# Kernel tuning notes

Hardware: AMD Instinct MI355X
Metric: run time of the kernel (lower is better)

The kernel has to match this reference:

```python
import jax, jax.numpy as jnp
import numpy as np

S, B, T = 2048, 256, 48


def setup_inputs() -> dict:
    key = jax.random.key(0)
    k1, k2, k3, k4 = jax.random.split(key, 4)
    emissions = jax.random.normal(k1, (S, B, T), dtype=jnp.float32)
    tags = jax.random.randint(k2, (S, B), 0, T, dtype=jnp.int64)
    mask = jnp.ones((S, B), dtype=jnp.int32)
    # params initialized uniform(-0.1, 0.1) as in reset_parameters
    start_transitions = jax.random.uniform(k3, (T,), minval=-0.1, maxval=0.1, dtype=jnp.float32)
    end_transitions = jax.random.uniform(k4, (T,), minval=-0.1, maxval=0.1, dtype=jnp.float32)
    transitions = jax.random.uniform(jax.random.fold_in(key, 7), (T, T), minval=-0.1, maxval=0.1, dtype=jnp.float32)
    return {
        "emissions": emissions,
        "tags": tags,
        "mask": mask,
        "start_transitions": start_transitions,
        "end_transitions": end_transitions,
        "transitions": transitions,
    }


def _compute_score(emissions, tags, mask, start_transitions, end_transitions, transitions):
    # emissions: (S,B,T), tags/mask: (S,B)
    seq_length, batch_size = tags.shape
    maskf = mask.astype(emissions.dtype)
    ar = jnp.arange(batch_size)
    # emission score of the chosen tag at every step: (S,B)
    em_scores = jnp.take_along_axis(emissions, tags[..., None], axis=2)[..., 0]
    score = start_transitions[tags[0]] + em_scores[0]
    # transition scores between consecutive tags, masked: (S-1,B)
    trans_scores = transitions[tags[:-1], tags[1:]] * maskf[1:]
    score = score + trans_scores.sum(axis=0) + (em_scores[1:] * maskf[1:]).sum(axis=0)
    seq_ends = mask.astype(jnp.int32).sum(axis=0) - 1  # (B,)
    last_tags = tags[seq_ends, ar]
    score = score + end_transitions[last_tags]
    return score  # (B,)


def _compute_normalizer(emissions, mask, start_transitions, end_transitions, transitions):
    # forward algorithm via lax.scan over time
    score0 = start_transitions + emissions[0]  # (B,T)

    def step(score, inp):
        em_i, m_i = inp  # (B,T), (B,)
        # (B, T_prev, T_next)
        next_score = jax.nn.logsumexp(score[:, :, None] + transitions[None, :, :] + em_i[:, None, :], axis=1)
        score = jnp.where(m_i[:, None] != 0, next_score, score)
        return score, None

    score, _ = jax.lax.scan(step, score0, (emissions[1:], mask[1:]))
    score = score + end_transitions
    return jax.nn.logsumexp(score, axis=1)  # (B,)


def reference(emissions, tags, mask, start_transitions, end_transitions, transitions):
    numerator = _compute_score(emissions, tags, mask, start_transitions, end_transitions, transitions)
    denominator = _compute_normalizer(emissions, mask, start_transitions, end_transitions, transitions)
    llh = numerator - denominator
    return llh.sum()  # reduction='sum'
```

## Files before the change

### kernel.cpp

```cpp
#include <hip/hip_runtime.h>
#include <hip/hip_bf16.h>
#include <math.h>

#define S_LEN  2048
#define B_SZ   256
#define T_TAGS 48
#define MAT_U32 1152

#define WS_CNT_OFF 0
#define WS_K_OFF   1024
#define WS_P_OFF   65536

using short8 = __attribute__((ext_vector_type(8))) short;
using f32x4  = __attribute__((ext_vector_type(4))) float;

__device__ __forceinline__ unsigned cvtpk(float lo, float hi) {
    unsigned r;
    asm("v_cvt_pk_bf16_f32 %0, %1, %2" : "=v"(r) : "v"(lo), "v"(hi));
    return r;
}

template<int CCH>
__global__ __launch_bounds__(64, 4) void crf_chunk_kernel(
    const float* __restrict__ em, const int* __restrict__ mask,
    const float* __restrict__ trans, unsigned* __restrict__ wsP,
    int* __restrict__ wsK, int* __restrict__ wsCnt)
{
    constexpr int LCH = S_LEN / CCH;
    constexpr int NQ  = LCH / 64;
    const int bid = blockIdx.x;
    const int b = bid / CCH, c = bid % CCH;
    const int tid = threadIdx.x;
    const int cc = tid & 15, g = tid >> 4;
    const int start = c * LCH;

    __shared__ __align__(16) uint4 lds4[384];
    char* Lc = (char*)lds4;

#pragma unroll
    for (int i = 0; i < 6; ++i) lds4[tid + 64 * i] = make_uint4(0u, 0u, 0u, 0u);
    __builtin_amdgcn_wave_barrier();
    if (tid < T_TAGS)
        *(unsigned short*)(Lc + (tid >> 4) * 2048 +
                           ((tid >> 3) * 16 + (tid & 15)) * 16 + (tid & 7) * 2) = 0x3F80;
    __builtin_amdgcn_wave_barrier();

    short8 Afr[3][2];
#pragma unroll
    for (int jt = 0; jt < 3; ++jt) {
        const int j = jt * 16 + cc;
#pragma unroll
        for (int kt = 0; kt < 2; ++kt) {
            unsigned u[4];
#pragma unroll
            for (int h = 0; h < 4; ++h) {
                const int k0 = kt * 32 + g * 8 + 2 * h;
                const float lo = (k0     < T_TAGS) ? __expf(trans[k0 * T_TAGS + j]) : 0.f;
                const float hi = (k0 + 1 < T_TAGS) ? __expf(trans[(k0 + 1) * T_TAGS + j]) : 0.f;
                u[h] = cvtpk(lo, hi);
            }
            uint4 uu = make_uint4(u[0], u[1], u[2], u[3]);
            Afr[jt][kt] = *reinterpret_cast<short8*>(&uu);
        }
    }

    unsigned long long ball[NQ];
    int cnt = 0;
#pragma unroll
    for (int q = 0; q < NQ; ++q) {
        const int s = start + q * 64 + tid;
        ball[q] = __ballot(mask[s * B_SZ + b] != 0);
        cnt += (int)__popcll(ball[q]);
    }
    if (tid == 0) atomicAdd(&wsCnt[b], cnt);
    if (c == 0) ball[0] &= ~1ull;

    int K = 0, pend = 0;
    float pscale = 1.0f;
    const f32x4 fz = {0.f, 0.f, 0.f, 0.f};
    const size_t embase = (size_t)b * T_TAGS + 4 * g;

    auto emload = [&](int t, f32x4& d0, f32x4& d1, f32x4& d2) {
        int ss = start + t; if (ss > S_LEN - 1) ss = S_LEN - 1;
        const float* p = em + (size_t)ss * (B_SZ * T_TAGS) + embase;
        d0 = *(const f32x4*)(p);
        d1 = *(const f32x4*)(p + 16);
        d2 = *(const f32x4*)(p + 32);
    };

    auto step = [&](bool on, const f32x4& e0, const f32x4& e1, const f32x4& e2) {
        if (!on) return;
        const short8 B00 = *(const short8*)(Lc +        tid * 16);
        const short8 B01 = *(const short8*)(Lc + 1024 + tid * 16);
        const short8 B10 = *(const short8*)(Lc + 2048 + tid * 16);
        const short8 B11 = *(const short8*)(Lc + 3072 + tid * 16);
        const short8 B20 = *(const short8*)(Lc + 4096 + tid * 16);
        const short8 B21 = *(const short8*)(Lc + 5120 + tid * 16);
        const float ps = pscale;
        float ef0[4], ef1[4], ef2[4];
#pragma unroll
        for (int r = 0; r < 4; ++r) {
            ef0[r] = __expf(e0[r]) * ps;
            ef1[r] = __expf(e1[r]) * ps;
            ef2[r] = __expf(e2[r]) * ps;
        }
        f32x4 z;
#define DOFRAG(JT, NT, BN0, BN1, EF, PROBE_)                                   \
        z = __builtin_amdgcn_mfma_f32_16x16x32_bf16(Afr[JT][0], BN0, fz, 0, 0, 0); \
        z = __builtin_amdgcn_mfma_f32_16x16x32_bf16(Afr[JT][1], BN1, z,  0, 0, 0); \
        if (PROBE_) {                                                          \
            const unsigned pb_ = (unsigned)__builtin_amdgcn_readfirstlane(     \
                (int)__float_as_uint(z[0]));                                   \
            const int ee_ = (int)((pb_ >> 23) & 255u);                         \
            const int kk_ = ee_ - 127;                                         \
            K += kk_; pend = kk_;                                              \
            pscale = __uint_as_float((unsigned)(254 - ee_) << 23);             \
        }                                                                      \
        *(uint2*)(Lc + (NT) * 2048 + ((2 * (JT) + (g >> 1)) * 16 + cc) * 16 +  \
                  (g & 1) * 8) =                                               \
            make_uint2(cvtpk(z[0] * EF[0], z[1] * EF[1]),                      \
                       cvtpk(z[2] * EF[2], z[3] * EF[3]))

        DOFRAG(0, 0, B00, B01, ef0, true);
        DOFRAG(0, 1, B10, B11, ef0, false);
        DOFRAG(0, 2, B20, B21, ef0, false);
        DOFRAG(1, 0, B00, B01, ef1, false);
        DOFRAG(1, 1, B10, B11, ef1, false);
        DOFRAG(1, 2, B20, B21, ef1, false);
        DOFRAG(2, 0, B00, B01, ef2, false);
        DOFRAG(2, 1, B10, B11, ef2, false);
        DOFRAG(2, 2, B20, B21, ef2, false);
#undef DOFRAG
    };

    f32x4 a0, a1, a2, b0, b1, b2;
    emload(0, a0, a1, a2);
    emload(1, b0, b1, b2);

#pragma unroll
    for (int q = 0; q < NQ; ++q) {
        const unsigned long long bq = ball[q];
        for (int tt = 0; tt < 64; tt += 2) {
            const int t = q * 64 + tt;
            step(((bq >> tt) & 1ull) != 0, a0, a1, a2);
            emload(t + 2, a0, a1, a2);
            step(((bq >> (tt + 1)) & 1ull) != 0, b0, b1, b2);
            emload(t + 3, b0, b1, b2);
        }
    }

    if (tid < T_TAGS) {
        unsigned w[24];
#pragma unroll
        for (int p = 0; p < 24; ++p) {
            const int i0 = 2 * p, i1 = i0 + 1;
            const unsigned lo = *(const unsigned short*)(Lc + (i0 >> 4) * 2048 +
                ((tid >> 3) * 16 + (i0 & 15)) * 16 + (tid & 7) * 2);
            const unsigned hi = *(const unsigned short*)(Lc + (i1 >> 4) * 2048 +
                ((tid >> 3) * 16 + (i1 & 15)) * 16 + (tid & 7) * 2);
            w[p] = lo | (hi << 16);
        }
        const unsigned base = (unsigned)bid * MAT_U32 + (unsigned)tid * 24;
#pragma unroll
        for (int qq = 0; qq < 6; ++qq)
            *reinterpret_cast<uint4*>(&wsP[base + 4 * qq]) =
                make_uint4(w[4 * qq], w[4 * qq + 1], w[4 * qq + 2], w[4 * qq + 3]);
    }
    if (tid == 0) wsK[bid] = K - pend;
}

template<int CCH>
__global__ __launch_bounds__(64, 1) void crf_combine_kernel(
    const float* __restrict__ em, const float* __restrict__ startT,
    const float* __restrict__ endT, const unsigned* __restrict__ wsP,
    const int* __restrict__ wsK, const int* __restrict__ wsCnt,
    const int* __restrict__ tags, float* __restrict__ out)
{
    const int b = blockIdx.x, tid = threadIdx.x;
    const int j = (tid < T_TAGS) ? tid : 0;
    float v = (tid < T_TAGS) ? __expf(startT[j] + em[(size_t)b * T_TAGS + j]) : 0.f;
    int K2 = 0;
    for (int c = 0; c < CCH; ++c) {
        const unsigned base = (unsigned)(b * CCH + c) * MAT_U32 + j * 24;
        uint4 W[6];
#pragma unroll
        for (int q = 0; q < 6; ++q)
            W[q] = *reinterpret_cast<const uint4*>(&wsP[base + 4 * q]);
        float a0 = 0.f, a1 = 0.f;
#pragma unroll
        for (int q = 0; q < 6; ++q) {
            const unsigned wv[4] = {W[q].x, W[q].y, W[q].z, W[q].w};
#pragma unroll
            for (int r = 0; r < 4; ++r) {
                const int i = q * 8 + r * 2;
                const float p0 = __uint_as_float(wv[r] << 16);
                const float p1 = __uint_as_float(wv[r] & 0xFFFF0000u);
                a0 = fmaf(__uint_as_float(__builtin_amdgcn_readlane(__float_as_uint(v), i)), p0, a0);
                a1 = fmaf(__uint_as_float(__builtin_amdgcn_readlane(__float_as_uint(v), i + 1)), p1, a1);
            }
        }
        const float vn = a0 + a1;
        const unsigned pb = (unsigned)__builtin_amdgcn_readfirstlane((int)__float_as_uint(vn));
        const int ee = (int)((pb >> 23) & 255u);
        const float sc = __uint_as_float((unsigned)(254 - ee) << 23);
        v = vn * sc;
        K2 += (ee - 127) + wsK[b * CCH + c];
    }
    float contrib = (tid < T_TAGS) ? v * __expf(endT[j]) : 0.f;
#pragma unroll
    for (int off = 32; off > 0; off >>= 1) contrib += __shfl_down(contrib, off);
    if (tid == 0) {
        const int cnt  = wsCnt[b];
        const int last = tags[(size_t)(cnt - 1) * B_SZ + b];
        const double den = (double)K2 * 0.6931471805599453 + (double)__logf(contrib);
        atomicAdd(out, endT[last] + (float)(-den));
    }
}

__global__ void crf_num_kernel(
    const float* __restrict__ em, const int* __restrict__ tags,
    const int* __restrict__ mask, const float* __restrict__ startT,
    const float* __restrict__ trans, float* __restrict__ out)
{
    const int N = S_LEN * B_SZ;
    float acc = 0.f;
    for (int idx = blockIdx.x * blockDim.x + threadIdx.x; idx < N;
         idx += gridDim.x * blockDim.x) {
        const int t = tags[idx];
        const float e = em[(size_t)idx * T_TAGS + t];
        if (idx < B_SZ) {
            acc += e + startT[t];
        } else if (mask[idx] != 0) {
            acc += e + trans[tags[idx - B_SZ] * T_TAGS + t];
        }
    }
#pragma unroll
    for (int off = 32; off > 0; off >>= 1)
        acc += __shfl_down(acc, off);
    if ((threadIdx.x & 63) == 0) atomicAdd(out, acc);
}

extern "C" void kernel_launch(void* const* d_in, const int* in_sizes, int n_in,
                              void* d_out, int out_size, void* d_ws, size_t ws_size,
                              hipStream_t stream)
{
    const float* em     = (const float*)d_in[0];
    const int*   tags   = (const int*)  d_in[1];
    const int*   mask   = (const int*)  d_in[2];
    const float* startT = (const float*)d_in[3];
    const float* endT   = (const float*)d_in[4];
    const float* trans  = (const float*)d_in[5];
    float* out = (float*)d_out;

    int*      wsCnt = (int*)((char*)d_ws + WS_CNT_OFF);
    int*      wsK   = (int*)((char*)d_ws + WS_K_OFF);
    unsigned* wsP   = (unsigned*)((char*)d_ws + WS_P_OFF);

    hipMemsetAsync(out, 0, sizeof(float), stream);
    hipMemsetAsync(wsCnt, 0, B_SZ * sizeof(int), stream);

    const size_t need16 = (size_t)WS_P_OFF + (size_t)(B_SZ * 16) * (MAT_U32 * 4);
    if (ws_size >= need16) {
        crf_chunk_kernel<16><<<B_SZ * 16, 64, 0, stream>>>(em, mask, trans, wsP, wsK, wsCnt);
        crf_num_kernel<<<512, 256, 0, stream>>>(em, tags, mask, startT, trans, out);
        crf_combine_kernel<16><<<B_SZ, 64, 0, stream>>>(em, startT, endT, wsP, wsK, wsCnt, tags, out);
    } else {
        crf_chunk_kernel<8><<<B_SZ * 8, 64, 0, stream>>>(em, mask, trans, wsP, wsK, wsCnt);
        crf_num_kernel<<<512, 256, 0, stream>>>(em, tags, mask, startT, trans, out);
        crf_combine_kernel<8><<<B_SZ, 64, 0, stream>>>(em, startT, endT, wsP, wsK, wsCnt, tags, out);
    }
}
```

Measured before the change: 226.8 us.

## Fuse numerator into chunk kernel, transpose via MFMA, add 32-chunk split

Computes the gold-path score inside the chunk kernel using the mask ballots already loaded, so the separate numerator kernel and its launch go away. Replaces the scalar LDS gather used to write the chunk matrix with identity-matrix MFMAs that transpose the fragments into registers before storing. Adds a 32-chunk-per-batch path when the workspace is large enough, doubling parallelism but also doubling the matrices the combine kernel must fold serially. The extra gathers in the chunk kernel and the heavier combine stage could offset the gains.

```diff
diff --git a/kernel.cpp b/kernel.cpp
--- a/kernel.cpp
+++ b/kernel.cpp
@@ -19,12 +19,17 @@
     asm("v_cvt_pk_bf16_f32 %0, %1, %2" : "=v"(r) : "v"(lo), "v"(hi));
     return r;
 }
+__device__ __forceinline__ unsigned pk2bf(float lo, float hi) {
+    __hip_bfloat162 h2 = __float22bfloat162_rn(make_float2(lo, hi));
+    return *reinterpret_cast<unsigned*>(&h2);
+}
 
 template<int CCH>
 __global__ __launch_bounds__(64, 4) void crf_chunk_kernel(
     const float* __restrict__ em, const int* __restrict__ mask,
-    const float* __restrict__ trans, unsigned* __restrict__ wsP,
-    int* __restrict__ wsK, int* __restrict__ wsCnt)
+    const float* __restrict__ trans, const int* __restrict__ tags,
+    const float* __restrict__ startT, unsigned* __restrict__ wsP,
+    int* __restrict__ wsK, int* __restrict__ wsCnt, float* __restrict__ out)
 {
     constexpr int LCH = S_LEN / CCH;
     constexpr int NQ  = LCH / 64;
@@ -45,6 +50,36 @@
                            ((tid >> 3) * 16 + (tid & 15)) * 16 + (tid & 7) * 2) = 0x3F80;
     __builtin_amdgcn_wave_barrier();
 
+    unsigned long long ball[NQ];
+    int cnt = 0;
+#pragma unroll
+    for (int q = 0; q < NQ; ++q) {
+        const int s = start + q * 64 + tid;
+        ball[q] = __ballot(mask[s * B_SZ + b] != 0);
+        cnt += (int)__popcll(ball[q]);
+    }
+    if (tid == 0) atomicAdd(&wsCnt[b], cnt);
+    if (c == 0) ball[0] &= ~1ull;
+
+    {
+        float nacc = 0.f;
+#pragma unroll
+        for (int q = 0; q < NQ; ++q) {
+            const int s = start + q * 64 + tid;
+            if (s == 0) {
+                const int t0 = tags[b];
+                nacc += em[(size_t)b * T_TAGS + t0] + startT[t0];
+            } else if ((ball[q] >> tid) & 1ull) {
+                const int tc = tags[(size_t)s * B_SZ + b];
+                const int tp = tags[(size_t)(s - 1) * B_SZ + b];
+                nacc += em[((size_t)s * B_SZ + b) * T_TAGS + tc] + trans[tp * T_TAGS + tc];
+            }
+        }
+#pragma unroll
+        for (int off = 32; off > 0; off >>= 1) nacc += __shfl_down(nacc, off);
+        if (tid == 0) atomicAdd(out, nacc);
+    }
+
     short8 Afr[3][2];
 #pragma unroll
     for (int jt = 0; jt < 3; ++jt) {
@@ -63,17 +98,6 @@
             Afr[jt][kt] = *reinterpret_cast<short8*>(&uu);
         }
     }
-
-    unsigned long long ball[NQ];
-    int cnt = 0;
-#pragma unroll
-    for (int q = 0; q < NQ; ++q) {
-        const int s = start + q * 64 + tid;
-        ball[q] = __ballot(mask[s * B_SZ + b] != 0);
-        cnt += (int)__popcll(ball[q]);
-    }
-    if (tid == 0) atomicAdd(&wsCnt[b], cnt);
-    if (c == 0) ball[0] &= ~1ull;
 
     int K = 0, pend = 0;
     float pscale = 1.0f;
@@ -116,8 +140,8 @@
             K += kk_; pend = kk_;                                              \
             pscale = __uint_as_float((unsigned)(254 - ee_) << 23);             \
         }                                                                      \
-        *(uint2*)(Lc + (NT) * 2048 + ((2 * (JT) + (g >> 1)) * 16 + cc) * 16 +  \
-                  (g & 1) * 8) =                                               \
+        *(uint2*)(Lc + (NT) * 2048 +                                           \
+                  ((2 * (JT) + (g >> 1)) * 16 + cc) * 16 + (g & 1) * 8) =      \
             make_uint2(cvtpk(z[0] * EF[0], z[1] * EF[1]),                      \
                        cvtpk(z[2] * EF[2], z[3] * EF[3]))
 
@@ -149,22 +173,35 @@
         }
     }
 
-    if (tid < T_TAGS) {
-        unsigned w[24];
-#pragma unroll
-        for (int p = 0; p < 24; ++p) {
-            const int i0 = 2 * p, i1 = i0 + 1;
-            const unsigned lo = *(const unsigned short*)(Lc + (i0 >> 4) * 2048 +
-                ((tid >> 3) * 16 + (i0 & 15)) * 16 + (tid & 7) * 2);
-            const unsigned hi = *(const unsigned short*)(Lc + (i1 >> 4) * 2048 +
-                ((tid >> 3) * 16 + (i1 & 15)) * 16 + (tid & 7) * 2);
-            w[p] = lo | (hi << 16);
-        }
-        const unsigned base = (unsigned)bid * MAT_U32 + (unsigned)tid * 24;
-#pragma unroll
-        for (int qq = 0; qq < 6; ++qq)
-            *reinterpret_cast<uint4*>(&wsP[base + 4 * qq]) =
-                make_uint4(w[4 * qq], w[4 * qq + 1], w[4 * qq + 2], w[4 * qq + 3]);
+    auto mkI = [&](int shift) -> short8 {
+        const int e = cc + shift - 8 * g;
+        uint4 uu;
+        uu.x = (e == 0) ? 0x3F80u : (e == 1) ? 0x3F800000u : 0u;
+        uu.y = (e == 2) ? 0x3F80u : (e == 3) ? 0x3F800000u : 0u;
+        uu.z = (e == 4) ? 0x3F80u : (e == 5) ? 0x3F800000u : 0u;
+        uu.w = (e == 6) ? 0x3F80u : (e == 7) ? 0x3F800000u : 0u;
+        return *reinterpret_cast<short8*>(&uu);
+    };
+    const short8 I0  = mkI(0);
+    const short8 I16 = mkI(16);
+
+    short8 F0[3], F1[3];
+#pragma unroll
+    for (int nt = 0; nt < 3; ++nt) {
+        F0[nt] = *(const short8*)(Lc + nt * 2048 +        tid * 16);
+        F1[nt] = *(const short8*)(Lc + nt * 2048 + 1024 + tid * 16);
+    }
+#pragma unroll
+    for (int nt = 0; nt < 3; ++nt) {
+#pragma unroll
+        for (int ct = 0; ct < 3; ++ct) {
+            const short8 Af = (ct < 2) ? F0[nt] : F1[nt];
+            const short8 Bi = (ct == 1) ? I16 : I0;
+            f32x4 z = __builtin_amdgcn_mfma_f32_16x16x32_bf16(Af, Bi, fz, 0, 0, 0);
+            const int jcol = ct * 16 + cc;
+            *(uint2*)&wsP[(size_t)bid * MAT_U32 + jcol * 24 + nt * 8 + g * 2] =
+                make_uint2(pk2bf(z[0], z[1]), pk2bf(z[2], z[3]));
+        }
     }
     if (tid == 0) wsK[bid] = K - pend;
 }
@@ -217,29 +254,6 @@
     }
 }
 
-__global__ void crf_num_kernel(
-    const float* __restrict__ em, const int* __restrict__ tags,
-    const int* __restrict__ mask, const float* __restrict__ startT,
-    const float* __restrict__ trans, float* __restrict__ out)
-{
-    const int N = S_LEN * B_SZ;
-    float acc = 0.f;
-    for (int idx = blockIdx.x * blockDim.x + threadIdx.x; idx < N;
-         idx += gridDim.x * blockDim.x) {
-        const int t = tags[idx];
-        const float e = em[(size_t)idx * T_TAGS + t];
-        if (idx < B_SZ) {
-            acc += e + startT[t];
-        } else if (mask[idx] != 0) {
-            acc += e + trans[tags[idx - B_SZ] * T_TAGS + t];
-        }
-    }
-#pragma unroll
-    for (int off = 32; off > 0; off >>= 1)
-        acc += __shfl_down(acc, off);
-    if ((threadIdx.x & 63) == 0) atomicAdd(out, acc);
-}
-
 extern "C" void kernel_launch(void* const* d_in, const int* in_sizes, int n_in,
                               void* d_out, int out_size, void* d_ws, size_t ws_size,
                               hipStream_t stream)
@@ -259,14 +273,16 @@
     hipMemsetAsync(out, 0, sizeof(float), stream);
     hipMemsetAsync(wsCnt, 0, B_SZ * sizeof(int), stream);
 
+    const size_t need32 = (size_t)WS_P_OFF + (size_t)(B_SZ * 32) * (MAT_U32 * 4);
     const size_t need16 = (size_t)WS_P_OFF + (size_t)(B_SZ * 16) * (MAT_U32 * 4);
-    if (ws_size >= need16) {
-        crf_chunk_kernel<16><<<B_SZ * 16, 64, 0, stream>>>(em, mask, trans, wsP, wsK, wsCnt);
-        crf_num_kernel<<<512, 256, 0, stream>>>(em, tags, mask, startT, trans, out);
+    if (ws_size >= need32) {
+        crf_chunk_kernel<32><<<B_SZ * 32, 64, 0, stream>>>(em, mask, trans, tags, startT, wsP, wsK, wsCnt, out);
+        crf_combine_kernel<32><<<B_SZ, 64, 0, stream>>>(em, startT, endT, wsP, wsK, wsCnt, tags, out);
+    } else if (ws_size >= need16) {
+        crf_chunk_kernel<16><<<B_SZ * 16, 64, 0, stream>>>(em, mask, trans, tags, startT, wsP, wsK, wsCnt, out);
         crf_combine_kernel<16><<<B_SZ, 64, 0, stream>>>(em, startT, endT, wsP, wsK, wsCnt, tags, out);
     } else {
-        crf_chunk_kernel<8><<<B_SZ * 8, 64, 0, stream>>>(em, mask, trans, wsP, wsK, wsCnt);
-        crf_num_kernel<<<512, 256, 0, stream>>>(em, tags, mask, startT, trans, out);
+        crf_chunk_kernel<8><<<B_SZ * 8, 64, 0, stream>>>(em, mask, trans, tags, startT, wsP, wsK, wsCnt, out);
         crf_combine_kernel<8><<<B_SZ, 64, 0, stream>>>(em, startT, endT, wsP, wsK, wsCnt, tags, out);
     }
 }
```

Result: slower. 257.9 us (+13.7%).
